# Kernel optimization log

Hardware: AMD Instinct MI355X
Metric: run time of the kernel (lower is better)

## Reference

```python
import jax, jax.numpy as jnp
import numpy as np

B, BOUNDS, NRIM, K, UNITS = 4096, 512, 6, 4, 600
H_IN, DK_IN, DV_IN = 4, 64, 400
H_C, DK_C, DV_C = 4, 32, 100


def setup_inputs() -> dict:
    key = jax.random.key(0)
    ks = jax.random.split(key, 16)
    s = 0.02
    return {
        'inputs': jax.random.normal(ks[0], (B, BOUNDS + NRIM), jnp.float32),
        'hs': jax.random.normal(ks[1], (B, NRIM, UNITS), jnp.float32) * s,
        'cs': jax.random.normal(ks[2], (B, NRIM, UNITS), jnp.float32) * s,
        'Wk': jax.random.normal(ks[3], (BOUNDS, H_IN * DK_IN), jnp.float32) * s,
        'bk': jnp.zeros((H_IN * DK_IN,), jnp.float32),
        'Wv': jax.random.normal(ks[4], (BOUNDS, H_IN * DV_IN), jnp.float32) * s,
        'bv': jnp.zeros((H_IN * DV_IN,), jnp.float32),
        'Wq': jax.random.normal(ks[5], (NRIM, UNITS, H_IN * DK_IN), jnp.float32) * s,
        'lstm_k': jax.random.normal(ks[6], (NRIM, DV_IN, 4 * UNITS), jnp.float32) * s,
        'lstm_r': jax.random.normal(ks[7], (NRIM, UNITS, 4 * UNITS), jnp.float32) * s,
        'lstm_b': jnp.zeros((NRIM, 4 * UNITS), jnp.float32),
        'Wkc': jax.random.normal(ks[8], (NRIM, UNITS, H_C * DK_C), jnp.float32) * s,
        'Wvc': jax.random.normal(ks[9], (NRIM, UNITS, H_C * DV_C), jnp.float32) * s,
        'Wqc': jax.random.normal(ks[10], (NRIM, UNITS, H_C * DK_C), jnp.float32) * s,
        'Wout': jax.random.normal(ks[11], (NRIM, H_C * DV_C, UNITS), jnp.float32) * s,
    }


def _split_heads(t, n_heads, d_head):
    # [B, T, n_heads*d_head] -> [B, n_heads, T, d_head] (matches tf.split+stack)
    b, t_len = t.shape[0], t.shape[1]
    return t.reshape(b, t_len, n_heads, d_head).transpose(0, 2, 1, 3)


def reference(inputs, hs, cs, Wk, bk, Wv, bv, Wq, lstm_k, lstm_r, lstm_b, Wkc, Wvc, Wqc, Wout):
    x = inputs[:, :BOUNDS]                                   # [B, bounds]
    rim_dist = inputs[:, BOUNDS:BOUNDS + NRIM]               # [B, nRIM]

    # ---- input attention ----
    xx = jnp.stack([x, jnp.zeros_like(x)], axis=1)           # [B, 2, bounds]
    k_lay = xx @ Wk + bk                                     # [B, 2, H*dk]
    v_lay = xx @ Wv + bv                                     # [B, 2, H*dv]
    q_lay = jnp.einsum('bnu,nuo->bno', hs, Wq)               # grouped linear [B, nRIM, H*dq]
    kh = _split_heads(k_lay, H_IN, DK_IN)                    # [B, H, 2, dk]
    vh = _split_heads(v_lay, H_IN, DV_IN)                    # [B, H, 2, dv]
    qh = _split_heads(q_lay, H_IN, DK_IN)                    # [B, H, nRIM, dk]
    v2 = vh.mean(axis=1)                                     # [B, 2, dv]
    scores = jnp.einsum('bhnd,bhtd->bhnt', qh, kh) / np.sqrt(DK_IN).astype(np.float32)
    scores2 = scores.mean(axis=1)                            # [B, nRIM, 2]

    # top-k RIM selection mask from RIM_dist (use_attn=False path)
    _, idx = jax.lax.top_k(rim_dist, K)                      # [B, K]
    mask = jnp.zeros((inputs.shape[0], NRIM), inputs.dtype)
    mask = mask.at[jnp.arange(inputs.shape[0])[:, None], idx].set(1.0)[..., None]  # [B, nRIM, 1]

    probs = jax.nn.softmax(scores2, axis=-1)                 # dropout inactive (training=False)
    rnn_in = jnp.einsum('bnt,btv->bnv', probs, v2) * mask    # [B, nRIM, dv]

    # ---- grouped LSTM (keras gate order i,f,c,o) ----
    gates = (jnp.einsum('bnv,nvo->bno', rnn_in, lstm_k)
             + jnp.einsum('bnu,nuo->bno', hs, lstm_r) + lstm_b)  # [B, nRIM, 4*units]
    i, f, g, o = jnp.split(gates, 4, axis=-1)
    c_rnn = jax.nn.sigmoid(f) * cs + jax.nn.sigmoid(i) * jnp.tanh(g)
    h_rnn = jax.nn.sigmoid(o) * jnp.tanh(c_rnn)
    h_new = jax.lax.stop_gradient(h_rnn * (1.0 - mask)) + h_rnn * mask

    # ---- communication attention among RIMs ----
    kc = _split_heads(jnp.einsum('bnu,nuo->bno', h_new, Wkc), H_C, DK_C)  # [B, Hc, nRIM, dkc]
    vc = _split_heads(jnp.einsum('bnu,nuo->bno', h_new, Wvc), H_C, DV_C)
    qc = _split_heads(jnp.einsum('bnu,nuo->bno', h_new, Wqc), H_C, DK_C)
    sc = jnp.einsum('bhnd,bhmd->bhnm', qc, kc) / np.sqrt(DK_C).astype(np.float32)
    pc = jax.nn.softmax(sc, axis=-1) * mask[:, None, :, :]   # zero rows of inactive query RIMs
    ctx = jnp.einsum('bhnm,bhmv->bhnv', pc, vc)              # [B, Hc, nRIM, dvc]
    ctx = ctx.transpose(0, 2, 1, 3).reshape(inputs.shape[0], NRIM, H_C * DV_C)
    h_comm = jnp.einsum('bno,nou->bnu', ctx, Wout) + h_new   # grouped output proj + residual

    # ---- masked state update ----
    h_upd = h_comm * mask + hs * (1.0 - mask)
    c_upd = c_rnn * mask + cs * (1.0 - mask)
    out_state = h_upd.reshape(inputs.shape[0], UNITS * NRIM)
    return out_state, h_upd, c_upd
```

## Files before the change

### kernel.cpp

```cpp
#include <hip/hip_runtime.h>

namespace {
typedef unsigned short u16;
typedef __attribute__((ext_vector_type(8))) __bf16 bf16x8;
typedef __attribute__((ext_vector_type(4))) float f32x4;

constexpr long long kB  = 4096;
constexpr long long kOS = kB * 3600;
constexpr size_t kGAs = 4096ull * 1024;

constexpr size_t oWkvT  = 0;
constexpr size_t oWqT   = oWkvT  + 768ull*512*2;
constexpr size_t oWcomT = oWqT   + 6ull*256*608*2;
constexpr size_t oWoutT = oWcomT + 6ull*768*608*2;
constexpr size_t oLstmT = oWoutT + 6ull*640*416*2;
constexpr size_t oBp    = oLstmT + 6ull*2432*1024*2;
constexpr size_t oBkv   = oBp    + 6ull*2432*4;
constexpr size_t oMask  = oBkv   + 768*4;
constexpr size_t oArena = oMask  + 4096ull*6*4;
constexpr size_t oGA    = oArena;
constexpr size_t oKV    = oGA   + 6ull*kGAs*2;
constexpr size_t oXbf   = oKV   + 4096ull*768*2;
constexpr size_t oQlay  = oXbf;
constexpr size_t oCqv   = oArena;
constexpr size_t oCtx   = oCqv  + 4096ull*4608*2;
}

__device__ __forceinline__ u16 f2b(float f) {
  union { float f; unsigned u; } x; x.f = f;
  unsigned r = (x.u + 0x7fffu + ((x.u >> 16) & 1u)) >> 16;
  return (u16)r;
}
__device__ __forceinline__ float b2f(u16 u) {
  union { unsigned u; float f; } x; x.u = ((unsigned)u) << 16;
  return x.f;
}
__device__ __forceinline__ float sigmoidf_(float x) { return 1.f / (1.f + __expf(-x)); }
__device__ __forceinline__ float tanhf_(float x) {
  const float e = __expf(2.f * x);
  return 1.f - 2.f / (e + 1.f);
}

__device__ __forceinline__ void gload16(const void* g, void* l) {
  __builtin_amdgcn_global_load_lds((const __attribute__((address_space(1))) void*)g,
                                   (__attribute__((address_space(3))) void*)l, 16, 0, 0);
}

union FragU { uint2 u2[2]; bf16x8 v; };
union FragU4 { uint4 u4; bf16x8 v; };

template<int MODE>
__global__ __launch_bounds__(256) void gemm128(
    const u16* __restrict__ A, int lda, long strideA,
    const u16* __restrict__ Bt, long strideB, int Kpad,
    void* __restrict__ C, int ldc, int strideC,
    const float* __restrict__ bias, int strideBias,
    int N, int nks, int storeBf16, int nx,
    const float* __restrict__ mask, float* __restrict__ h_upd,
    const float* __restrict__ hs_in, float* __restrict__ out_state)
{
  __shared__ __align__(16) u16 As[128 * 32];
  __shared__ __align__(16) u16 Bs[128 * 32];

  const int nwg = gridDim.x;
  const int orig = blockIdx.x;
  const int q = nwg >> 3, r = nwg & 7;
  const int xcd = orig & 7, bidx = orig >> 3;
  const int wgid = (xcd < r ? xcd * (q + 1) : r * (q + 1) + (xcd - r) * q) + bidx;
  const int xt = wgid % nx;
  const int t2 = wgid / nx;
  const int mt = t2 & 31;
  const int rim = t2 >> 5;
  const int m0 = mt * 128, n0 = xt * 128;

  A += (size_t)rim * strideA;
  Bt += (size_t)rim * strideB;
  if (bias) bias += (size_t)rim * strideBias;

  const int t = threadIdx.x;
  const int w = t >> 6, lane = t & 63;
  const int lrow = lane & 15, lk = lane >> 4;
  const int wr = w >> 1, wc = w & 1;

  f32x4 acc[4][4] = {};

  const int rA0 = t >> 2,         cA0 = (t & 3) ^ ((rA0 >> 1) & 3);
  const int rA1 = (t + 256) >> 2, cA1 = (t & 3) ^ ((rA1 >> 1) & 3);

  for (int s = 0; s < nks; ++s) {
    const int k0 = s * 32;
    {
      gload16(A + (size_t)(m0 + rA0) * lda + k0 + cA0 * 8, &As[(size_t)t * 8]);
      gload16(A + (size_t)(m0 + rA1) * lda + k0 + cA1 * 8, &As[(size_t)(t + 256) * 8]);
      gload16(Bt + (size_t)(n0 + rA0) * Kpad + k0 + cA0 * 8, &Bs[(size_t)t * 8]);
      gload16(Bt + (size_t)(n0 + rA1) * Kpad + k0 + cA1 * 8, &Bs[(size_t)(t + 256) * 8]);
    }
    __syncthreads();
    FragU af[4], bfr[4];
#pragma unroll
    for (int mf = 0; mf < 4; ++mf) {
      const int rr = wr * 64 + mf * 16 + lrow;
      const int sw = ((rr >> 1) & 3) << 4;
      const char* base = (const char*)As + rr * 64;
      af[mf].u2[0] = *(const uint2*)(base + ((8 * lk) ^ sw));
      af[mf].u2[1] = *(const uint2*)(base + ((8 * lk + 32) ^ sw));
    }
#pragma unroll
    for (int nf = 0; nf < 4; ++nf) {
      const int rr = wc * 64 + nf * 16 + lrow;
      const int sw = ((rr >> 1) & 3) << 4;
      const char* base = (const char*)Bs + rr * 64;
      bfr[nf].u2[0] = *(const uint2*)(base + ((8 * lk) ^ sw));
      bfr[nf].u2[1] = *(const uint2*)(base + ((8 * lk + 32) ^ sw));
    }
#pragma unroll
    for (int mf = 0; mf < 4; ++mf)
#pragma unroll
      for (int nf = 0; nf < 4; ++nf)
        acc[mf][nf] = __builtin_amdgcn_mfma_f32_16x16x32_bf16(af[mf].v, bfr[nf].v, acc[mf][nf], 0, 0, 0);
    __syncthreads();
  }

  if (MODE == 0) {
    float* Cf = (float*)C + (size_t)rim * strideC;
    u16*   Cu = (u16*)C + (size_t)rim * strideC;
#pragma unroll
    for (int mf = 0; mf < 4; ++mf)
#pragma unroll
      for (int r2 = 0; r2 < 4; ++r2) {
        const int m = m0 + wr * 64 + mf * 16 + 4 * lk + r2;
#pragma unroll
        for (int nf = 0; nf < 4; ++nf) {
          const int col = n0 + wc * 64 + nf * 16 + lrow;
          if (col < N) {
            float v = acc[mf][nf][r2];
            if (bias) v += bias[col];
            const size_t off = (size_t)m * ldc + col;
            if (storeBf16) Cu[off] = f2b(v); else Cf[off] = v;
          }
        }
      }
  } else {
#pragma unroll
    for (int mf = 0; mf < 4; ++mf)
#pragma unroll
      for (int r2 = 0; r2 < 4; ++r2) {
        const int m = m0 + wr * 64 + mf * 16 + 4 * lk + r2;
        const float mk = mask[(size_t)m * 6 + rim];
#pragma unroll
        for (int nf = 0; nf < 4; ++nf) {
          const int col = n0 + wc * 64 + nf * 16 + lrow;
          if (col < 600) {
            const size_t off = (size_t)m * 3600 + rim * 600 + col;
            const float v = (mk != 0.f) ? (acc[mf][nf][r2] + h_upd[off]) : hs_in[off];
            h_upd[off] = v;
            out_state[off] = v;
          }
        }
      }
  }
}

__global__ __launch_bounds__(512, 1) void gates8(
    const u16* __restrict__ A, const u16* __restrict__ Bt,
    const float* __restrict__ bp, const float* __restrict__ cs,
    const float* __restrict__ mask,
    float* __restrict__ c_upd, float* __restrict__ h_upd, u16* __restrict__ hnbf)
{
  __shared__ __align__(16) u16 lds[3 * 24576];

  const int nwg = gridDim.x;
  const int orig = blockIdx.x;
  const int q = nwg >> 3;
  const int xcd = orig & 7, bidx = orig >> 3;
  const int wgid = xcd * q + bidx;
  const int g = wgid / 160;
  const int rem = wgid % 160;
  const int rim = g >> 1;
  const int mt = rem / 10;
  const int ntl = (g & 1) * 10 + rem % 10;
  if (ntl >= 19) return;
  const int m0 = mt * 256, n0 = ntl * 128;

  const u16* Ar = A + (size_t)rim * kGAs;
  const u16* Br = Bt + (size_t)rim * (2432ull * 1024);

  const int t = threadIdx.x;
  const int w = t >> 6, lane = t & 63;
  const int lrow = lane & 15, lk = lane >> 4;
  const int wr = w >> 2, wc = w & 3;

  f32x4 acc[8][2] = {};

  auto stage = [&](int s, u16* dst) {
    const int k0 = s * 64;
#pragma unroll
    for (int i = 0; i < 4; ++i) {
      const int c = t + i * 512;
      const int row = c >> 3;
      const int gk = k0 + (((c & 7) ^ (row & 7)) << 3);
      gload16(Ar + (size_t)(m0 + row) * 1024 + gk, dst + (size_t)c * 8);
    }
#pragma unroll
    for (int i = 0; i < 2; ++i) {
      const int c = t + i * 512;
      const int row = c >> 3;
      const int gk = k0 + (((c & 7) ^ (row & 7)) << 3);
      gload16(Br + (size_t)(n0 + row) * 1024 + gk, dst + 16384 + (size_t)c * 8);
    }
  };

  constexpr int nks = 16;
  stage(0, lds);
  stage(1, lds + 24576);
  for (int s = 0; s < nks; ++s) {
    if (s == nks - 1) asm volatile("s_waitcnt vmcnt(0)" ::: "memory");
    else              asm volatile("s_waitcnt vmcnt(6)" ::: "memory");
    __builtin_amdgcn_s_barrier();
    __builtin_amdgcn_sched_barrier(0);
    if (s + 2 < nks) {
      int b2 = s + 2; b2 -= (b2 / 3) * 3;
      stage(s + 2, lds + b2 * 24576);
    }
    const u16* Ab = lds + (s % 3) * 24576;
    const u16* Bb = Ab + 16384;
#pragma unroll
    for (int ks = 0; ks < 2; ++ks) {
      FragU4 af[8], bf[2];
#pragma unroll
      for (int mf = 0; mf < 8; ++mf) {
        const int rr = wr * 128 + mf * 16 + lrow;
        const int byo = rr * 128 + ((((ks << 2) | lk) ^ (rr & 7)) << 4);
        af[mf].u4 = *(const uint4*)((const char*)Ab + byo);
      }
#pragma unroll
      for (int nf = 0; nf < 2; ++nf) {
        const int rr = wc * 32 + nf * 16 + lrow;
        const int byo = rr * 128 + ((((ks << 2) | lk) ^ (rr & 7)) << 4);
        bf[nf].u4 = *(const uint4*)((const char*)Bb + byo);
      }
#pragma unroll
      for (int mf = 0; mf < 8; ++mf)
#pragma unroll
        for (int nf = 0; nf < 2; ++nf)
          acc[mf][nf] = __builtin_amdgcn_mfma_f32_16x16x32_bf16(af[mf].v, bf[nf].v, acc[mf][nf], 0, 0, 0);
    }
  }

  __builtin_amdgcn_s_barrier();
  float* ex = (float*)lds;
#pragma unroll
  for (int mf = 0; mf < 8; ++mf)
#pragma unroll
    for (int nf = 0; nf < 2; ++nf)
#pragma unroll
      for (int r2 = 0; r2 < 4; ++r2) {
        const int rr = wr * 128 + mf * 16 + 4 * lk + r2;
        const int col = wc * 32 + nf * 16 + lrow;
        ex[rr * 132 + col] = acc[mf][nf][r2];
      }
  __builtin_amdgcn_s_barrier();

  const int u = t & 31;
  const int rb = (t >> 5) * 16;
  const int au = ntl * 32 + u;
  if (au < 600) {
    const int ci = ((u >> 4) << 6) + (u & 15);
    const float b_i = bp[rim * 2432 + n0 + ci];
    const float b_f = bp[rim * 2432 + n0 + ci + 16];
    const float b_g = bp[rim * 2432 + n0 + ci + 32];
    const float b_o = bp[rim * 2432 + n0 + ci + 48];
#pragma unroll 4
    for (int rr2 = 0; rr2 < 16; ++rr2) {
      const int rloc = rb + rr2;
      const int m = m0 + rloc;
      const float iv = ex[rloc * 132 + ci] + b_i;
      const float fv = ex[rloc * 132 + ci + 16] + b_f;
      const float gv = ex[rloc * 132 + ci + 32] + b_g;
      const float ov = ex[rloc * 132 + ci + 48] + b_o;
      const size_t off = (size_t)m * 3600 + rim * 600 + au;
      const float cprev = cs[off];
      const float cv = sigmoidf_(fv) * cprev + sigmoidf_(iv) * tanhf_(gv);
      const float hv = sigmoidf_(ov) * tanhf_(cv);
      const float mk = mask[(size_t)m * 6 + rim];
      c_upd[off] = (mk != 0.f) ? cv : cprev;
      h_upd[off] = hv;
      hnbf[off]  = f2b(hv);
    }
  }
}

__device__ void pack_wt_body(float (*tile)[65], int bx, int by, int rim,
    const float* __restrict__ i1, long s1, const float* __restrict__ i2, long s2,
    int K1, int Ktot, int ldin, int Nreal,
    u16* __restrict__ out, long so, int Kpad, int gateperm, int tid)
{
  i1 += (size_t)rim * s1;
  if (i2) i2 += (size_t)rim * s2;
  u16* o = out + (size_t)rim * so;
  const int n0 = bx * 64, k0 = by * 64;
  const int lane = tid & 63, qq = tid >> 6;
  const int n = n0 + lane;
  int col;
  if (gateperm) {
    const int g = (n >> 4) & 3, u = ((n >> 6) << 4) + (n & 15);
    col = (u < 600) ? g * 600 + u : -1;
  } else {
    col = (n < Nreal) ? n : -1;
  }
#pragma unroll
  for (int i = 0; i < 16; ++i) {
    const int kk = qq + 4 * i;
    const int k = k0 + kk;
    float v = 0.f;
    if (col >= 0) {
      if (k < K1) v = i1[(size_t)k * ldin + col];
      else if (k < Ktot) v = i2[(size_t)(k - K1) * ldin + col];
    }
    tile[kk][lane] = v;
  }
  __syncthreads();
#pragma unroll
  for (int i = 0; i < 16; ++i) {
    const int nn = qq + 4 * i;
    const int k = k0 + lane;
    if (k < Kpad) o[(size_t)(n0 + nn) * Kpad + k] = f2b(tile[lane][nn]);
  }
}

__global__ __launch_bounds__(256) void megapack_w(
    const float* __restrict__ Wk, const float* __restrict__ Wv,
    const float* __restrict__ Wkc, const float* __restrict__ Wqc, const float* __restrict__ Wvc,
    const float* __restrict__ Wq, const float* __restrict__ Wout,
    const float* __restrict__ lstm_k, const float* __restrict__ lstm_r,
    u16* __restrict__ WkvT, u16* __restrict__ WcomT, u16* __restrict__ WqT,
    u16* __restrict__ WoutT, u16* __restrict__ LstmT)
{
  __shared__ float tile[64][65];
  const int id = blockIdx.x, t = threadIdx.x;
  if (id < 3648) {
    const int bx = id % 38, by = (id / 38) % 16, bz = id / 608;
    pack_wt_body(tile, bx, by, bz, lstm_k, 400l*2400, lstm_r, 600l*2400,
                 400, 1000, 2400, 2400, LstmT, 2432l*1024, 1024, 1, t);
  } else if (id < 4068) {
    const int i2 = id - 3648;
    const int bx = i2 % 10, by = (i2 / 10) % 7, bz = i2 / 70;
    pack_wt_body(tile, bx, by, bz, Wout, 400l*600, nullptr, 0,
                 400, 400, 600, 600, WoutT, 640l*416, 416, 0, t);
  } else if (id < 4308) {
    const int i3 = id - 4068;
    const int bx = i3 % 4, by = (i3 / 4) % 10, bz = i3 / 40;
    pack_wt_body(tile, bx, by, bz, Wq, 600l*256, nullptr, 0,
                 600, 600, 256, 256, WqT, 256l*608, 608, 0, t);
  } else if (id < 4500) {
    const int e8 = ((id - 4308) * 256 + t) * 8;
    const int n = e8 >> 9, k0 = e8 & 511;
    u16 st[8];
#pragma unroll
    for (int j = 0; j < 8; ++j) {
      const int k = k0 + j;
      float v = 0.f;
      if (n < 256) v = Wk[(size_t)k * 256 + n];
      else if (n < 656) {
        const float* p = Wv + (size_t)k * 1600 + (n - 256);
        v = 0.25f * (p[0] + p[400] + p[800] + p[1200]);
      }
      st[j] = f2b(v);
    }
    *(uint4*)(WkvT + e8) = *(const uint4*)st;
  } else {
    const long long e8 = ((long long)(id - 4500) * 256 + t) * 8;
    const int rim = (int)(e8 / 466944);
    const int rem = (int)(e8 % 466944);
    const int n = rem / 608, k0 = rem % 608;
    u16 st[8];
#pragma unroll
    for (int j = 0; j < 8; ++j) {
      const int k = k0 + j;
      float v = 0.f;
      if (k < 600) {
        if (n < 128)      v = Wkc[(size_t)rim * 76800 + (size_t)k * 128 + n];
        else if (n < 256) v = Wqc[(size_t)rim * 76800 + (size_t)k * 128 + (n - 128)];
        else if (n < 656) v = Wvc[(size_t)rim * 240000 + (size_t)k * 400 + (n - 256)];
      }
      st[j] = f2b(v);
    }
    *(uint4*)(WcomT + e8) = *(const uint4*)st;
  }
}

__global__ __launch_bounds__(256) void megapack_act(
    const float* __restrict__ inputs, const float* __restrict__ hs,
    const float* __restrict__ lstm_b, const float* __restrict__ bk, const float* __restrict__ bv,
    u16* __restrict__ xbf, u16* __restrict__ gA, float* __restrict__ bp, float* __restrict__ bkv)
{
  __shared__ float row[3600];
  const int id = blockIdx.x, t = threadIdx.x;
  if (id < 4096) {
    const int b = id;
    for (int i = t; i < 3600; i += 256) row[i] = hs[(size_t)b * 3600 + i];
    __syncthreads();
    for (int c = t; c < 468; c += 256) {
      const int rim = c / 78;
      const int j = (c % 78) * 8;
      u16 v[8];
#pragma unroll
      for (int k = 0; k < 8; ++k) {
        const int col = j + k;
        v[k] = (col < 600) ? f2b(row[rim * 600 + col]) : (u16)0;
      }
      *(uint4*)(gA + (size_t)rim * kGAs + (size_t)b * 1024 + 400 + j) = *(const uint4*)v;
    }
  } else if (id < 5120) {
    const int e8 = ((id - 4096) * 256 + t) * 8;
    const int b = e8 >> 9, c0 = e8 & 511;
    const float* src = inputs + (size_t)b * 518 + c0;
    u16 st[8];
#pragma unroll
    for (int j = 0; j < 8; ++j) st[j] = f2b(src[j]);
    *(uint4*)(xbf + e8) = *(const uint4*)st;
  } else {
    const int tt = (id - 5120) * 256 + t;
    if (tt < 6 * 2432) {
      const int rim = tt / 2432, p = tt % 2432;
      const int g = (p >> 4) & 3, u = ((p >> 6) << 4) + (p & 15);
      bp[tt] = (u < 600) ? lstm_b[(size_t)rim * 2400 + g * 600 + u] : 0.f;
    }
    if (tt < 768) {
      float v = 0.f;
      if (tt < 256) v = bk[tt];
      else if (tt < 656) { const int j2 = tt - 256; v = 0.25f * (bv[j2] + bv[j2+400] + bv[j2+800] + bv[j2+1200]); }
      bkv[tt] = v;
    }
  }
}

__global__ __launch_bounds__(256) void score_kernel(
    const float* __restrict__ inputs, const u16* __restrict__ qlayb,
    const u16* __restrict__ kvb, const float* __restrict__ bk,
    const float* __restrict__ bkv,
    float* __restrict__ maskout, u16* __restrict__ gA)
{
  const int b = blockIdx.x;
  const int t = threadIdx.x;
  __shared__ float red[4][12];
  __shared__ float sprob[12];
  __shared__ float smask[6];

  const float k0v = b2f(kvb[(size_t)b * 768 + t]);
  const float bkv_ = bk[t];
  float part[12];
#pragma unroll
  for (int n = 0; n < 6; ++n) {
    const float q = b2f(qlayb[(size_t)b * 1536 + n * 256 + t]);
    part[2 * n]     = q * k0v;
    part[2 * n + 1] = q * bkv_;
  }
#pragma unroll
  for (int off = 32; off > 0; off >>= 1)
#pragma unroll
    for (int i = 0; i < 12; ++i)
      part[i] += __shfl_down(part[i], off);
  const int wave = t >> 6, lane = t & 63;
  if (lane == 0)
#pragma unroll
    for (int i = 0; i < 12; ++i) red[wave][i] = part[i];
  __syncthreads();
  if (t < 12) red[0][t] = (red[0][t] + red[1][t] + red[2][t] + red[3][t]) * (1.0f / 32.0f);
  __syncthreads();
  if (t < 6) {
    const float s0 = red[0][2 * t], s1 = red[0][2 * t + 1];
    const float mx = fmaxf(s0, s1);
    const float e0 = __expf(s0 - mx), e1 = __expf(s1 - mx);
    const float inv = 1.f / (e0 + e1);
    sprob[2 * t] = e0 * inv;
    sprob[2 * t + 1] = e1 * inv;
    const float* rd = inputs + (size_t)b * 518 + 512;
    const float mine = rd[t];
    int rank = 0;
#pragma unroll
    for (int j = 0; j < 6; ++j) {
      const float o = rd[j];
      rank += (o > mine) || (o == mine && j < t);
    }
    const float mk = (rank < 4) ? 1.f : 0.f;
    smask[t] = mk;
    maskout[(size_t)b * 6 + t] = mk;
  }
  __syncthreads();
  for (int c = t; c < 300; c += 256) {
    const int n = c / 50;
    const int v = (c % 50) * 8;
    const float p0 = sprob[2 * n], p1 = sprob[2 * n + 1], mk = smask[n];
    u16 st[8];
#pragma unroll
    for (int k = 0; k < 8; ++k)
      st[k] = f2b((p0 * b2f(kvb[(size_t)b * 768 + 256 + v + k]) + p1 * bkv[256 + v + k]) * mk);
    *reinterpret_cast<uint4*>(gA + (size_t)n * kGAs + (size_t)b * 1024 + v) =
        *reinterpret_cast<const uint4*>(st);
  }
}

__global__ __launch_bounds__(256) void comm_kernel(
    const u16* __restrict__ cqv, u16* __restrict__ ctx)
{
  const int b = blockIdx.x, t = threadIdx.x;
  __shared__ float skc[768], sqc[768], svc[2400];
  __shared__ float spc[4][6][6];
  for (int i = t * 4; i < 4608; i += 1024) {
    const ushort4 u4 = *reinterpret_cast<const ushort4*>(cqv + (size_t)b * 4608 + i);
    const u16 uu[4] = {u4.x, u4.y, u4.z, u4.w};
#pragma unroll
    for (int j = 0; j < 4; ++j) {
      const int ii = i + j;
      const int m = ii / 768, c = ii % 768;
      const float v = b2f(uu[j]);
      if (c < 128) skc[m * 128 + c] = v;
      else if (c < 256) sqc[m * 128 + (c - 128)] = v;
      else if (c < 656) svc[m * 400 + (c - 256)] = v;
    }
  }
  __syncthreads();
  if (t < 144) {
    const int h = t / 36, n = (t % 36) / 6, m = t % 6;
    float s = 0.f;
#pragma unroll
    for (int d = 0; d < 32; ++d) s += sqc[n * 128 + h * 32 + d] * skc[m * 128 + h * 32 + d];
    spc[h][n][m] = s * 0.17677669529663687f;
  }
  __syncthreads();
  if (t < 24) {
    const int h = t / 6, n = t % 6;
    float mx = -3.0e38f;
#pragma unroll
    for (int m = 0; m < 6; ++m) mx = fmaxf(mx, spc[h][n][m]);
    float e[6], sum = 0.f;
#pragma unroll
    for (int m = 0; m < 6; ++m) { e[m] = __expf(spc[h][n][m] - mx); sum += e[m]; }
    const float inv = 1.f / sum;
#pragma unroll
    for (int m = 0; m < 6; ++m) spc[h][n][m] = e[m] * inv;
  }
  __syncthreads();
  for (int base = t * 4; base < 2400; base += 1024) {
    const int n = base / 400, rr = base % 400, h = rr / 100, v = rr % 100;
    ushort4 st;
    float s0 = 0.f, s1 = 0.f, s2 = 0.f, s3 = 0.f;
#pragma unroll
    for (int m = 0; m < 6; ++m) {
      const float p = spc[h][n][m];
      const float* vm = &svc[m * 400 + h * 100 + v];
      s0 += p * vm[0]; s1 += p * vm[1]; s2 += p * vm[2]; s3 += p * vm[3];
    }
    st.x = f2b(s0); st.y = f2b(s1); st.z = f2b(s2); st.w = f2b(s3);
    *reinterpret_cast<ushort4*>(ctx + (size_t)b * 2400 + base) = st;
  }
}

extern "C" void kernel_launch(void* const* d_in, const int* in_sizes, int n_in,
                              void* d_out, int out_size, void* d_ws, size_t ws_size,
                              hipStream_t stream) {
  const float* inputs = (const float*)d_in[0];
  const float* hs     = (const float*)d_in[1];
  const float* cs     = (const float*)d_in[2];
  const float* Wk     = (const float*)d_in[3];
  const float* bk     = (const float*)d_in[4];
  const float* Wv     = (const float*)d_in[5];
  const float* bv     = (const float*)d_in[6];
  const float* Wq     = (const float*)d_in[7];
  const float* lstm_k = (const float*)d_in[8];
  const float* lstm_r = (const float*)d_in[9];
  const float* lstm_b = (const float*)d_in[10];
  const float* Wkc    = (const float*)d_in[11];
  const float* Wvc    = (const float*)d_in[12];
  const float* Wqc    = (const float*)d_in[13];
  const float* Wout   = (const float*)d_in[14];

  float* out = (float*)d_out;
  float* out_state = out;
  float* h_upd = out + kOS;
  float* c_upd = out + 2 * kOS;
  u16*   hnbf  = (u16*)d_out;

  char* wsb = (char*)d_ws;
  u16* WkvT  = (u16*)(wsb + oWkvT);
  u16* WqT   = (u16*)(wsb + oWqT);
  u16* WcomT = (u16*)(wsb + oWcomT);
  u16* WoutT = (u16*)(wsb + oWoutT);
  u16* LstmT = (u16*)(wsb + oLstmT);
  float* bp    = (float*)(wsb + oBp);
  float* bkv   = (float*)(wsb + oBkv);
  float* maskf = (float*)(wsb + oMask);
  u16* gA    = (u16*)(wsb + oGA);
  u16* kvb   = (u16*)(wsb + oKV);
  u16* xbf   = (u16*)(wsb + oXbf);
  u16* qlayb = (u16*)(wsb + oQlay);
  u16* cqvb  = (u16*)(wsb + oCqv);
  u16* ctxb  = (u16*)(wsb + oCtx);

  dim3 B256(256);

  megapack_w<<<5868, B256, 0, stream>>>(Wk, Wv, Wkc, Wqc, Wvc, Wq, Wout, lstm_k, lstm_r,
                                        WkvT, WcomT, WqT, WoutT, LstmT);
  megapack_act<<<5177, B256, 0, stream>>>(inputs, hs, lstm_b, bk, bv, xbf, gA, bp, bkv);

  gemm128<0><<<dim3(192), B256, 0, stream>>>(xbf, 512, 0, WkvT, 0, 512,
      kvb, 768, 0, bkv, 0, 656, 16, 1, 6, nullptr, nullptr, nullptr, nullptr);
  gemm128<0><<<dim3(384), B256, 0, stream>>>(gA + 400, 1024, (long)kGAs, WqT, 256l*608, 608,
      qlayb, 1536, 256, nullptr, 0, 256, 19, 1, 2, nullptr, nullptr, nullptr, nullptr);

  score_kernel<<<4096, B256, 0, stream>>>(inputs, qlayb, kvb, bk, bkv, maskf, gA);

  gates8<<<dim3(1920), dim3(512), 0, stream>>>(gA, LstmT, bp, cs, maskf, c_upd, h_upd, hnbf);

  gemm128<0><<<dim3(1152), B256, 0, stream>>>(hnbf, 3600, 600, WcomT, 768l*608, 608,
      cqvb, 4608, 768, nullptr, 0, 656, 19, 1, 6, nullptr, nullptr, nullptr, nullptr);

  comm_kernel<<<4096, B256, 0, stream>>>(cqvb, ctxb);

  gemm128<1><<<dim3(960), B256, 0, stream>>>(ctxb, 2400, 400, WoutT, 640l*416, 416,
      nullptr, 0, 0, nullptr, 0, 600, 13, 0, 5, maskf, h_upd, hs, out_state);
}
```

Before: 626.1 us.

## Unify GEMMs into double-buffered K64 kernel and fold LSTM gates into it

Replaces the single-buffered K=32 gemm128 with a gemm64 kernel. It loads K=64 slabs into a double-buffered, XOR-swizzled LDS layout so the next stage's global-to-LDS load overlaps the current MFMAs. The separate 256x128 triple-buffered gates8 kernel is removed, and the LSTM gate GEMM plus its nonlinearity epilogue now run as a MODE 2 specialisation of the same kernel with 128x128 tiles and two blocks per CU. Weight and activation padding strides grow to multiples of 64 (608→640, 416→448, 1024→1088 row stride) to fit the new K step. The trade-off is less register reuse per tile and a shallower pipeline for the dominant gate GEMM, plus extra padded loads.

```diff
diff --git a/kernel.cpp b/kernel.cpp
--- a/kernel.cpp
+++ b/kernel.cpp
@@ -7,13 +7,13 @@
 
 constexpr long long kB  = 4096;
 constexpr long long kOS = kB * 3600;
-constexpr size_t kGAs = 4096ull * 1024;
+constexpr size_t kGAs = 4096ull * 1088;
 
 constexpr size_t oWkvT  = 0;
 constexpr size_t oWqT   = oWkvT  + 768ull*512*2;
-constexpr size_t oWcomT = oWqT   + 6ull*256*608*2;
-constexpr size_t oWoutT = oWcomT + 6ull*768*608*2;
-constexpr size_t oLstmT = oWoutT + 6ull*640*416*2;
+constexpr size_t oWcomT = oWqT   + 6ull*256*640*2;
+constexpr size_t oWoutT = oWcomT + 6ull*768*640*2;
+constexpr size_t oLstmT = oWoutT + 6ull*640*448*2;
 constexpr size_t oBp    = oLstmT + 6ull*2432*1024*2;
 constexpr size_t oBkv   = oBp    + 6ull*2432*4;
 constexpr size_t oMask  = oBkv   + 768*4;
@@ -46,31 +46,39 @@
                                    (__attribute__((address_space(3))) void*)l, 16, 0, 0);
 }
 
-union FragU { uint2 u2[2]; bf16x8 v; };
 union FragU4 { uint4 u4; bf16x8 v; };
 
 template<int MODE>
-__global__ __launch_bounds__(256) void gemm128(
+__global__ __launch_bounds__(256, 2) void gemm64(
     const u16* __restrict__ A, int lda, long strideA,
     const u16* __restrict__ Bt, long strideB, int Kpad,
     void* __restrict__ C, int ldc, int strideC,
     const float* __restrict__ bias, int strideBias,
-    int N, int nks, int storeBf16, int nx,
-    const float* __restrict__ mask, float* __restrict__ h_upd,
+    int N, int nks, int storeBf16, int nx, int swz,
+    const float* __restrict__ cs, const float* __restrict__ mask,
+    float* __restrict__ c_upd, float* __restrict__ h_upd, u16* __restrict__ hnbf,
     const float* __restrict__ hs_in, float* __restrict__ out_state)
 {
-  __shared__ __align__(16) u16 As[128 * 32];
-  __shared__ __align__(16) u16 Bs[128 * 32];
+  __shared__ __align__(16) u16 lds[2 * 16384];
 
   const int nwg = gridDim.x;
   const int orig = blockIdx.x;
-  const int q = nwg >> 3, r = nwg & 7;
-  const int xcd = orig & 7, bidx = orig >> 3;
-  const int wgid = (xcd < r ? xcd * (q + 1) : r * (q + 1) + (xcd - r) * q) + bidx;
-  const int xt = wgid % nx;
-  const int t2 = wgid / nx;
-  const int mt = t2 & 31;
-  const int rim = t2 >> 5;
+  int wgid;
+  {
+    const int q = nwg >> 3, r = nwg & 7;
+    const int xcd = orig & 7, bidx = orig >> 3;
+    wgid = (xcd < r ? xcd * (q + 1) : r * (q + 1) + (xcd - r) * q) + bidx;
+  }
+  int mt, rim, xt;
+  if (swz == 1) {
+    const int g = wgid / 320, rem = wgid % 320;
+    rim = g >> 1; mt = rem / 10; xt = (g & 1) * 10 + rem % 10;
+    if (xt >= 19) return;
+  } else {
+    xt = wgid % nx;
+    const int t2 = wgid / nx;
+    mt = t2 & 31; rim = t2 >> 5;
+  }
   const int m0 = mt * 128, n0 = xt * 128;
 
   A += (size_t)rim * strideA;
@@ -84,41 +92,57 @@
 
   f32x4 acc[4][4] = {};
 
-  const int rA0 = t >> 2,         cA0 = (t & 3) ^ ((rA0 >> 1) & 3);
-  const int rA1 = (t + 256) >> 2, cA1 = (t & 3) ^ ((rA1 >> 1) & 3);
+  const u16* aS[4]; const u16* bS[4]; int cC[4];
+#pragma unroll
+  for (int i = 0; i < 4; ++i) {
+    const int c = t + i * 256;
+    const int row = c >> 3, slot = c & 7;
+    cC[i] = c;
+    aS[i] = A  + (size_t)(m0 + row) * lda  + ((slot ^ (row & 7)) << 3);
+    bS[i] = Bt + (size_t)(n0 + row) * Kpad + ((slot ^ (row & 7)) << 3);
+  }
+  auto stage = [&](u16* dst) {
+#pragma unroll
+    for (int i = 0; i < 4; ++i) gload16(aS[i], dst + (size_t)cC[i] * 8);
+#pragma unroll
+    for (int i = 0; i < 4; ++i) gload16(bS[i], dst + 8192 + (size_t)cC[i] * 8);
+#pragma unroll
+    for (int i = 0; i < 4; ++i) { aS[i] += 64; bS[i] += 64; }
+  };
+
+  stage(lds);
+  asm volatile("s_waitcnt vmcnt(0)" ::: "memory");
+  __builtin_amdgcn_s_barrier();
 
   for (int s = 0; s < nks; ++s) {
-    const int k0 = s * 32;
-    {
-      gload16(A + (size_t)(m0 + rA0) * lda + k0 + cA0 * 8, &As[(size_t)t * 8]);
-      gload16(A + (size_t)(m0 + rA1) * lda + k0 + cA1 * 8, &As[(size_t)(t + 256) * 8]);
-      gload16(Bt + (size_t)(n0 + rA0) * Kpad + k0 + cA0 * 8, &Bs[(size_t)t * 8]);
-      gload16(Bt + (size_t)(n0 + rA1) * Kpad + k0 + cA1 * 8, &Bs[(size_t)(t + 256) * 8]);
-    }
-    __syncthreads();
-    FragU af[4], bfr[4];
-#pragma unroll
-    for (int mf = 0; mf < 4; ++mf) {
-      const int rr = wr * 64 + mf * 16 + lrow;
-      const int sw = ((rr >> 1) & 3) << 4;
-      const char* base = (const char*)As + rr * 64;
-      af[mf].u2[0] = *(const uint2*)(base + ((8 * lk) ^ sw));
-      af[mf].u2[1] = *(const uint2*)(base + ((8 * lk + 32) ^ sw));
-    }
-#pragma unroll
-    for (int nf = 0; nf < 4; ++nf) {
-      const int rr = wc * 64 + nf * 16 + lrow;
-      const int sw = ((rr >> 1) & 3) << 4;
-      const char* base = (const char*)Bs + rr * 64;
-      bfr[nf].u2[0] = *(const uint2*)(base + ((8 * lk) ^ sw));
-      bfr[nf].u2[1] = *(const uint2*)(base + ((8 * lk + 32) ^ sw));
-    }
-#pragma unroll
-    for (int mf = 0; mf < 4; ++mf)
-#pragma unroll
-      for (int nf = 0; nf < 4; ++nf)
-        acc[mf][nf] = __builtin_amdgcn_mfma_f32_16x16x32_bf16(af[mf].v, bfr[nf].v, acc[mf][nf], 0, 0, 0);
-    __syncthreads();
+    const bool more = (s + 1 < nks);
+    if (more) stage(lds + ((s + 1) & 1) * 16384);
+    __builtin_amdgcn_sched_barrier(0);
+    const char* Ab = (const char*)(lds + (s & 1) * 16384);
+    const char* Bb = Ab + 16384;
+#pragma unroll
+    for (int ks = 0; ks < 2; ++ks) {
+      FragU4 af[4], bf4[4];
+#pragma unroll
+      for (int mf = 0; mf < 4; ++mf) {
+        const int rr = wr * 64 + mf * 16 + lrow;
+        af[mf].u4 = *(const uint4*)(Ab + rr * 128 + ((((ks << 2) | lk) ^ (rr & 7)) << 4));
+      }
+#pragma unroll
+      for (int nf = 0; nf < 4; ++nf) {
+        const int rr = wc * 64 + nf * 16 + lrow;
+        bf4[nf].u4 = *(const uint4*)(Bb + rr * 128 + ((((ks << 2) | lk) ^ (rr & 7)) << 4));
+      }
+#pragma unroll
+      for (int mf = 0; mf < 4; ++mf)
+#pragma unroll
+        for (int nf = 0; nf < 4; ++nf)
+          acc[mf][nf] = __builtin_amdgcn_mfma_f32_16x16x32_bf16(af[mf].v, bf4[nf].v, acc[mf][nf], 0, 0, 0);
+    }
+    if (more) {
+      asm volatile("s_waitcnt vmcnt(0)" ::: "memory");
+      __builtin_amdgcn_s_barrier();
+    }
   }
 
   if (MODE == 0) {
@@ -140,7 +164,7 @@
           }
         }
       }
-  } else {
+  } else if (MODE == 1) {
 #pragma unroll
     for (int mf = 0; mf < 4; ++mf)
 #pragma unroll
@@ -158,134 +182,32 @@
           }
         }
       }
-  }
-}
-
-__global__ __launch_bounds__(512, 1) void gates8(
-    const u16* __restrict__ A, const u16* __restrict__ Bt,
-    const float* __restrict__ bp, const float* __restrict__ cs,
-    const float* __restrict__ mask,
-    float* __restrict__ c_upd, float* __restrict__ h_upd, u16* __restrict__ hnbf)
-{
-  __shared__ __align__(16) u16 lds[3 * 24576];
-
-  const int nwg = gridDim.x;
-  const int orig = blockIdx.x;
-  const int q = nwg >> 3;
-  const int xcd = orig & 7, bidx = orig >> 3;
-  const int wgid = xcd * q + bidx;
-  const int g = wgid / 160;
-  const int rem = wgid % 160;
-  const int rim = g >> 1;
-  const int mt = rem / 10;
-  const int ntl = (g & 1) * 10 + rem % 10;
-  if (ntl >= 19) return;
-  const int m0 = mt * 256, n0 = ntl * 128;
-
-  const u16* Ar = A + (size_t)rim * kGAs;
-  const u16* Br = Bt + (size_t)rim * (2432ull * 1024);
-
-  const int t = threadIdx.x;
-  const int w = t >> 6, lane = t & 63;
-  const int lrow = lane & 15, lk = lane >> 4;
-  const int wr = w >> 2, wc = w & 3;
-
-  f32x4 acc[8][2] = {};
-
-  auto stage = [&](int s, u16* dst) {
-    const int k0 = s * 64;
-#pragma unroll
-    for (int i = 0; i < 4; ++i) {
-      const int c = t + i * 512;
-      const int row = c >> 3;
-      const int gk = k0 + (((c & 7) ^ (row & 7)) << 3);
-      gload16(Ar + (size_t)(m0 + row) * 1024 + gk, dst + (size_t)c * 8);
-    }
-#pragma unroll
-    for (int i = 0; i < 2; ++i) {
-      const int c = t + i * 512;
-      const int row = c >> 3;
-      const int gk = k0 + (((c & 7) ^ (row & 7)) << 3);
-      gload16(Br + (size_t)(n0 + row) * 1024 + gk, dst + 16384 + (size_t)c * 8);
-    }
-  };
-
-  constexpr int nks = 16;
-  stage(0, lds);
-  stage(1, lds + 24576);
-  for (int s = 0; s < nks; ++s) {
-    if (s == nks - 1) asm volatile("s_waitcnt vmcnt(0)" ::: "memory");
-    else              asm volatile("s_waitcnt vmcnt(6)" ::: "memory");
-    __builtin_amdgcn_s_barrier();
-    __builtin_amdgcn_sched_barrier(0);
-    if (s + 2 < nks) {
-      int b2 = s + 2; b2 -= (b2 / 3) * 3;
-      stage(s + 2, lds + b2 * 24576);
-    }
-    const u16* Ab = lds + (s % 3) * 24576;
-    const u16* Bb = Ab + 16384;
-#pragma unroll
-    for (int ks = 0; ks < 2; ++ks) {
-      FragU4 af[8], bf[2];
-#pragma unroll
-      for (int mf = 0; mf < 8; ++mf) {
-        const int rr = wr * 128 + mf * 16 + lrow;
-        const int byo = rr * 128 + ((((ks << 2) | lk) ^ (rr & 7)) << 4);
-        af[mf].u4 = *(const uint4*)((const char*)Ab + byo);
-      }
-#pragma unroll
-      for (int nf = 0; nf < 2; ++nf) {
-        const int rr = wc * 32 + nf * 16 + lrow;
-        const int byo = rr * 128 + ((((ks << 2) | lk) ^ (rr & 7)) << 4);
-        bf[nf].u4 = *(const uint4*)((const char*)Bb + byo);
-      }
-#pragma unroll
-      for (int mf = 0; mf < 8; ++mf)
-#pragma unroll
-        for (int nf = 0; nf < 2; ++nf)
-          acc[mf][nf] = __builtin_amdgcn_mfma_f32_16x16x32_bf16(af[mf].v, bf[nf].v, acc[mf][nf], 0, 0, 0);
-    }
-  }
-
-  __builtin_amdgcn_s_barrier();
-  float* ex = (float*)lds;
-#pragma unroll
-  for (int mf = 0; mf < 8; ++mf)
-#pragma unroll
-    for (int nf = 0; nf < 2; ++nf)
-#pragma unroll
-      for (int r2 = 0; r2 < 4; ++r2) {
-        const int rr = wr * 128 + mf * 16 + 4 * lk + r2;
-        const int col = wc * 32 + nf * 16 + lrow;
-        ex[rr * 132 + col] = acc[mf][nf][r2];
-      }
-  __builtin_amdgcn_s_barrier();
-
-  const int u = t & 31;
-  const int rb = (t >> 5) * 16;
-  const int au = ntl * 32 + u;
-  if (au < 600) {
-    const int ci = ((u >> 4) << 6) + (u & 15);
-    const float b_i = bp[rim * 2432 + n0 + ci];
-    const float b_f = bp[rim * 2432 + n0 + ci + 16];
-    const float b_g = bp[rim * 2432 + n0 + ci + 32];
-    const float b_o = bp[rim * 2432 + n0 + ci + 48];
-#pragma unroll 4
-    for (int rr2 = 0; rr2 < 16; ++rr2) {
-      const int rloc = rb + rr2;
-      const int m = m0 + rloc;
-      const float iv = ex[rloc * 132 + ci] + b_i;
-      const float fv = ex[rloc * 132 + ci + 16] + b_f;
-      const float gv = ex[rloc * 132 + ci + 32] + b_g;
-      const float ov = ex[rloc * 132 + ci + 48] + b_o;
-      const size_t off = (size_t)m * 3600 + rim * 600 + au;
-      const float cprev = cs[off];
-      const float cv = sigmoidf_(fv) * cprev + sigmoidf_(iv) * tanhf_(gv);
-      const float hv = sigmoidf_(ov) * tanhf_(cv);
-      const float mk = mask[(size_t)m * 6 + rim];
-      c_upd[off] = (mk != 0.f) ? cv : cprev;
-      h_upd[off] = hv;
-      hnbf[off]  = f2b(hv);
+  } else {
+    const int nb = n0 + wc * 64;
+    const int u = ((nb >> 6) << 4) + lrow;
+    if (u < 600) {
+      const float b_i = bias[nb + lrow];
+      const float b_f = bias[nb + 16 + lrow];
+      const float b_g = bias[nb + 32 + lrow];
+      const float b_o = bias[nb + 48 + lrow];
+#pragma unroll
+      for (int mf = 0; mf < 4; ++mf)
+#pragma unroll
+        for (int r2 = 0; r2 < 4; ++r2) {
+          const int m = m0 + wr * 64 + mf * 16 + 4 * lk + r2;
+          const float iv = acc[mf][0][r2] + b_i;
+          const float fv = acc[mf][1][r2] + b_f;
+          const float gv = acc[mf][2][r2] + b_g;
+          const float ov = acc[mf][3][r2] + b_o;
+          const size_t off = (size_t)m * 3600 + rim * 600 + u;
+          const float cprev = cs[off];
+          const float cv = sigmoidf_(fv) * cprev + sigmoidf_(iv) * tanhf_(gv);
+          const float hv = sigmoidf_(ov) * tanhf_(cv);
+          const float mk = mask[(size_t)m * 6 + rim];
+          c_upd[off] = (mk != 0.f) ? cv : cprev;
+          h_upd[off] = hv;
+          hnbf[off]  = f2b(hv);
+        }
     }
   }
 }
@@ -346,12 +268,12 @@
     const int i2 = id - 3648;
     const int bx = i2 % 10, by = (i2 / 10) % 7, bz = i2 / 70;
     pack_wt_body(tile, bx, by, bz, Wout, 400l*600, nullptr, 0,
-                 400, 400, 600, 600, WoutT, 640l*416, 416, 0, t);
+                 400, 400, 600, 600, WoutT, 640l*448, 448, 0, t);
   } else if (id < 4308) {
     const int i3 = id - 4068;
     const int bx = i3 % 4, by = (i3 / 4) % 10, bz = i3 / 40;
     pack_wt_body(tile, bx, by, bz, Wq, 600l*256, nullptr, 0,
-                 600, 600, 256, 256, WqT, 256l*608, 608, 0, t);
+                 600, 600, 256, 256, WqT, 256l*640, 640, 0, t);
   } else if (id < 4500) {
     const int e8 = ((id - 4308) * 256 + t) * 8;
     const int n = e8 >> 9, k0 = e8 & 511;
@@ -370,9 +292,9 @@
     *(uint4*)(WkvT + e8) = *(const uint4*)st;
   } else {
     const long long e8 = ((long long)(id - 4500) * 256 + t) * 8;
-    const int rim = (int)(e8 / 466944);
-    const int rem = (int)(e8 % 466944);
-    const int n = rem / 608, k0 = rem % 608;
+    const int rim = (int)(e8 / 491520);
+    const int rem = (int)(e8 % 491520);
+    const int n = rem / 640, k0 = rem % 640;
     u16 st[8];
 #pragma unroll
     for (int j = 0; j < 8; ++j) {
@@ -400,16 +322,16 @@
     const int b = id;
     for (int i = t; i < 3600; i += 256) row[i] = hs[(size_t)b * 3600 + i];
     __syncthreads();
-    for (int c = t; c < 468; c += 256) {
-      const int rim = c / 78;
-      const int j = (c % 78) * 8;
+    for (int c = t; c < 516; c += 256) {
+      const int rim = c / 86;
+      const int j = (c % 86) * 8;
       u16 v[8];
 #pragma unroll
       for (int k = 0; k < 8; ++k) {
         const int col = j + k;
         v[k] = (col < 600) ? f2b(row[rim * 600 + col]) : (u16)0;
       }
-      *(uint4*)(gA + (size_t)rim * kGAs + (size_t)b * 1024 + 400 + j) = *(const uint4*)v;
+      *(uint4*)(gA + (size_t)rim * kGAs + (size_t)b * 1088 + 400 + j) = *(const uint4*)v;
     }
   } else if (id < 5120) {
     const int e8 = ((id - 4096) * 256 + t) * 8;
@@ -496,7 +418,7 @@
 #pragma unroll
     for (int k = 0; k < 8; ++k)
       st[k] = f2b((p0 * b2f(kvb[(size_t)b * 768 + 256 + v + k]) + p1 * bkv[256 + v + k]) * mk);
-    *reinterpret_cast<uint4*>(gA + (size_t)n * kGAs + (size_t)b * 1024 + v) =
+    *reinterpret_cast<uint4*>(gA + (size_t)n * kGAs + (size_t)b * 1088 + v) =
         *reinterpret_cast<const uint4*>(st);
   }
 }
@@ -600,24 +522,30 @@
 
   dim3 B256(256);
 
-  megapack_w<<<5868, B256, 0, stream>>>(Wk, Wv, Wkc, Wqc, Wvc, Wq, Wout, lstm_k, lstm_r,
+  megapack_w<<<5940, B256, 0, stream>>>(Wk, Wv, Wkc, Wqc, Wvc, Wq, Wout, lstm_k, lstm_r,
                                         WkvT, WcomT, WqT, WoutT, LstmT);
   megapack_act<<<5177, B256, 0, stream>>>(inputs, hs, lstm_b, bk, bv, xbf, gA, bp, bkv);
 
-  gemm128<0><<<dim3(192), B256, 0, stream>>>(xbf, 512, 0, WkvT, 0, 512,
-      kvb, 768, 0, bkv, 0, 656, 16, 1, 6, nullptr, nullptr, nullptr, nullptr);
-  gemm128<0><<<dim3(384), B256, 0, stream>>>(gA + 400, 1024, (long)kGAs, WqT, 256l*608, 608,
-      qlayb, 1536, 256, nullptr, 0, 256, 19, 1, 2, nullptr, nullptr, nullptr, nullptr);
+  gemm64<0><<<dim3(192), B256, 0, stream>>>(xbf, 512, 0, WkvT, 0, 512,
+      kvb, 768, 0, bkv, 0, 656, 8, 1, 6, 0,
+      nullptr, nullptr, nullptr, nullptr, nullptr, nullptr, nullptr);
+  gemm64<0><<<dim3(384), B256, 0, stream>>>(gA + 400, 1088, (long)kGAs, WqT, 256l*640, 640,
+      qlayb, 1536, 256, nullptr, 0, 256, 10, 1, 2, 0,
+      nullptr, nullptr, nullptr, nullptr, nullptr, nullptr, nullptr);
 
   score_kernel<<<4096, B256, 0, stream>>>(inputs, qlayb, kvb, bk, bkv, maskf, gA);
 
-  gates8<<<dim3(1920), dim3(512), 0, stream>>>(gA, LstmT, bp, cs, maskf, c_upd, h_upd, hnbf);
-
-  gemm128<0><<<dim3(1152), B256, 0, stream>>>(hnbf, 3600, 600, WcomT, 768l*608, 608,
-      cqvb, 4608, 768, nullptr, 0, 656, 19, 1, 6, nullptr, nullptr, nullptr, nullptr);
+  gemm64<2><<<dim3(3840), B256, 0, stream>>>(gA, 1088, (long)kGAs, LstmT, 2432l*1024, 1024,
+      nullptr, 0, 0, bp, 2432, 2432, 16, 0, 0, 1,
+      cs, maskf, c_upd, h_upd, hnbf, nullptr, nullptr);
+
+  gemm64<0><<<dim3(1152), B256, 0, stream>>>(hnbf, 3600, 600, WcomT, 768l*640, 640,
+      cqvb, 4608, 768, nullptr, 0, 656, 10, 1, 6, 0,
+      nullptr, nullptr, nullptr, nullptr, nullptr, nullptr, nullptr);
 
   comm_kernel<<<4096, B256, 0, stream>>>(cqvb, ctxb);
 
-  gemm128<1><<<dim3(960), B256, 0, stream>>>(ctxb, 2400, 400, WoutT, 640l*416, 416,
-      nullptr, 0, 0, nullptr, 0, 600, 13, 0, 5, maskf, h_upd, hs, out_state);
-}
+  gemm64<1><<<dim3(960), B256, 0, stream>>>(ctxb, 2400, 400, WoutT, 640l*448, 448,
+      nullptr, 0, 0, nullptr, 0, 600, 7, 0, 5, 0,
+      nullptr, maskf, nullptr, h_upd, nullptr, hs, out_state);
+}
```

Result: faster. 578.5 us (-7.6%).
